# Performance work log

Measured on AMD Instinct MI355X. Metric: run time of the kernel, lower is better.

## Reference

```python
import jax, jax.numpy as jnp
import numpy as np

B, T, K, H = 8192, 96, 32, 768  # batch, max_len, output_dim (tags), bert hidden


def setup_inputs() -> dict:
    key = jax.random.key(0)
    k1, k2, k3, k4 = jax.random.split(key, 4)
    hidden = jax.random.normal(k1, (B, H), dtype=jnp.float32)
    target = jax.random.randint(k2, (B, T), 0, K, dtype=jnp.int32)
    # Dense(output_dim * max_len) params
    W = jax.random.normal(k3, (H, T * K), dtype=jnp.float32) * 0.02
    b = jnp.zeros((T * K,), dtype=jnp.float32)
    # tf.random.uniform transition matrix
    transitions = jax.random.uniform(k4, (K, K), dtype=jnp.float32)
    return {"hidden": hidden, "target": target, "W": W, "b": b, "transitions": transitions}


def _crf_log_norm(em_tm, transitions):
    # em_tm: [T, B, K] time-major emissions. Forward algorithm (logsumexp recurrence).
    def step(alpha, em_t):
        # alpha: [B, K]; broadcast over next-tag axis
        new = jax.nn.logsumexp(alpha[:, :, None] + transitions[None, :, :], axis=1) + em_t
        return new, None
    alpha, _ = jax.lax.scan(step, em_tm[0], em_tm[1:])
    return jax.nn.logsumexp(alpha, axis=-1)  # [B]


def _crf_sequence_score(em_btk, target, transitions):
    # unary: emission score at gold tags; binary: transition scores along gold path
    unary = jnp.take_along_axis(em_btk, target[..., None], axis=-1)[..., 0].sum(-1)
    binary = transitions[target[:, :-1], target[:, 1:]].sum(-1)
    return unary + binary  # [B]


def _viterbi_decode(em_tm, transitions):
    # em_tm: [T, B, K]. Max-product forward pass collecting backpointers.
    def fwd(v, em_t):
        scores = v[:, :, None] + transitions[None, :, :]  # [B, K_prev, K_next]
        bp = jnp.argmax(scores, axis=1).astype(jnp.int32)  # [B, K]
        return jnp.max(scores, axis=1) + em_t, bp
    v, bps = jax.lax.scan(fwd, em_tm[0], em_tm[1:])  # bps: [T-1, B, K]
    last_tag = jnp.argmax(v, axis=-1).astype(jnp.int32)  # [B]
    # backtrace (reverse scan); output index i is the tag at time i
    def back(tag, bp_t):
        prev = jnp.take_along_axis(bp_t, tag[:, None], axis=1)[:, 0]
        return prev, prev
    _, prevs = jax.lax.scan(back, last_tag, bps, reverse=True)  # [T-1, B]
    tags = jnp.concatenate([prevs, last_tag[None, :]], axis=0)  # [T, B]
    return jnp.transpose(tags), jnp.max(v, axis=-1)


def reference(hidden, target, W, b, transitions):
    # Dense with sigmoid, then reshape to (B, max_len, output_dim)
    em = jax.nn.sigmoid(hidden @ W + b).reshape(hidden.shape[0], T, K)
    em_tm = jnp.transpose(em, (1, 0, 2))  # time-major for scan
    log_likelihood = _crf_sequence_score(em, target, transitions) - _crf_log_norm(em_tm, transitions)
    decode_predict, _ = _viterbi_decode(em_tm, transitions)
    return decode_predict, log_likelihood
```

## Files before the change

### kernel.cpp

```cpp
#include <hip/hip_runtime.h>
#include <cstdint>
#include <cstddef>

#define B_  8192
#define T_  96
#define K_  32
#define H_  768
#define NK_ (T_ * K_)

typedef __attribute__((ext_vector_type(8))) _Float16 f16x8;
typedef __attribute__((ext_vector_type(4))) float    f32x4;

#define SCALE_UP   4096.0f
#define SCALE_DOWN (1.0f / 16777216.0f)

__device__ __forceinline__ void load_lds16(const void* g, void* l) {
    __builtin_amdgcn_global_load_lds(
        (const __attribute__((address_space(1))) unsigned int*)g,
        (__attribute__((address_space(3))) unsigned int*)l,
        16, 0, 0);
}

__global__ __launch_bounds__(256) void splitA_kernel(
    const float* __restrict__ A, _Float16* __restrict__ Ath, _Float16* __restrict__ Atl)
{
    const int g   = blockIdx.x * 256 + threadIdx.x;
    const int row = g / 96;
    const int o   = g - row * 96;
    const int ks  = o >> 2, qq = o & 3;
    const int r   = row & 127, rb = row >> 7;
    const size_t dst = (size_t)(rb * 24 + ks) * 4096 + r * 32 + ((qq ^ ((r >> 1) & 3)) << 3);

    f32x4 v0 = *(const f32x4*)(A + (size_t)row * H_ + o * 8);
    f32x4 v1 = *(const f32x4*)(A + (size_t)row * H_ + o * 8 + 4);
    f16x8 hi, lo;
#pragma unroll
    for (int e = 0; e < 8; e++) {
        float x = ((e < 4) ? v0[e] : v1[e - 4]) * SCALE_UP;
        _Float16 h = (_Float16)x;
        hi[e] = h;
        lo[e] = (_Float16)(x - (float)h);
    }
    *(f16x8*)&Ath[dst] = hi;
    *(f16x8*)&Atl[dst] = lo;
}

__global__ __launch_bounds__(256) void splitW_kernel(
    const float* __restrict__ W, _Float16* __restrict__ Wth, _Float16* __restrict__ Wtl)
{
    const int g   = blockIdx.x * 256 + threadIdx.x;
    const int ko  = g / NK_;
    const int col = g - ko * NK_;
    const int k0  = ko * 8;
    const int cb  = col >> 7, n = col & 127;
    const int ks  = k0 >> 5, qq = (k0 & 31) >> 3;
    const size_t dst = (size_t)(cb * 24 + ks) * 4096 + n * 32 + ((qq ^ ((n >> 1) & 3)) << 3);

    f16x8 hi, lo;
#pragma unroll
    for (int j = 0; j < 8; j++) {
        float x = W[(size_t)(k0 + j) * NK_ + col] * SCALE_UP;
        _Float16 h = (_Float16)x;
        hi[j] = h;
        lo[j] = (_Float16)(x - (float)h);
    }
    *(f16x8*)&Wth[dst] = hi;
    *(f16x8*)&Wtl[dst] = lo;
}

__global__ __launch_bounds__(256, 2) void gemm_mfma_sigmoid_kernel(
    const _Float16* __restrict__ Ath, const _Float16* __restrict__ Atl,
    const _Float16* __restrict__ Wth, const _Float16* __restrict__ Wtl,
    const float* __restrict__ bias, float* __restrict__ em)
{
    __shared__ _Float16 lds[2][4][4096];

    const int tid  = threadIdx.x;
    const int cb   = blockIdx.x;
    const int rb   = blockIdx.y;
    const int lane = tid & 63;
    const int w    = tid >> 6;
    const int wr   = w >> 1, wc = w & 1;
    const int fr   = lane & 15;
    const int kg   = lane >> 4;

    const _Float16* srcs[4] = {
        Ath + (size_t)(rb * 24) * 4096, Atl + (size_t)(rb * 24) * 4096,
        Wth + (size_t)(cb * 24) * 4096, Wtl + (size_t)(cb * 24) * 4096 };

    auto stage = [&](int ks, int bb) {
#pragma unroll
        for (int m = 0; m < 4; m++) {
            const _Float16* s = srcs[m] + (size_t)ks * 4096 + w * 1024 + lane * 8;
            _Float16* d = &lds[bb][m][w * 1024];
            load_lds16(s, d);
            load_lds16(s + 512, d + 512);
        }
    };

    f32x4 acc[4][4];
#pragma unroll
    for (int i = 0; i < 4; i++)
#pragma unroll
        for (int j = 0; j < 4; j++) acc[i][j] = (f32x4)0.0f;

    int cur = 0;
    stage(0, 0);

    for (int ks = 0; ks < 24; ks++) {
        __syncthreads();
        if (ks + 1 < 24) stage(ks + 1, cur ^ 1);

        f16x8 fah[4], fal[4], fbh[4], fbl[4];
#pragma unroll
        for (int mi = 0; mi < 4; mi++) {
            const int r   = wr * 64 + mi * 16 + fr;
            const int idx = r * 32 + ((kg ^ ((r >> 1) & 3)) << 3);
            fah[mi] = *(const f16x8*)&lds[cur][0][idx];
            fal[mi] = *(const f16x8*)&lds[cur][1][idx];
        }
#pragma unroll
        for (int ni = 0; ni < 4; ni++) {
            const int r   = wc * 64 + ni * 16 + fr;
            const int idx = r * 32 + ((kg ^ ((r >> 1) & 3)) << 3);
            fbh[ni] = *(const f16x8*)&lds[cur][2][idx];
            fbl[ni] = *(const f16x8*)&lds[cur][3][idx];
        }
#pragma unroll
        for (int mi = 0; mi < 4; mi++)
#pragma unroll
            for (int ni = 0; ni < 4; ni++) {
                acc[mi][ni] = __builtin_amdgcn_mfma_f32_16x16x32_f16(fah[mi], fbh[ni], acc[mi][ni], 0, 0, 0);
                acc[mi][ni] = __builtin_amdgcn_mfma_f32_16x16x32_f16(fah[mi], fbl[ni], acc[mi][ni], 0, 0, 0);
                acc[mi][ni] = __builtin_amdgcn_mfma_f32_16x16x32_f16(fal[mi], fbh[ni], acc[mi][ni], 0, 0, 0);
            }
        cur ^= 1;
    }

    const int er = rb * 128 + wr * 64 + (lane >> 4) * 4;
    const int ec = cb * 128 + wc * 64 + fr;
#pragma unroll
    for (int ni = 0; ni < 4; ni++) {
        const int   gc = ec + ni * 16;
        const float bv = bias[gc];
#pragma unroll
        for (int mi = 0; mi < 4; mi++)
#pragma unroll
            for (int r = 0; r < 4; r++) {
                const int gr = er + mi * 16 + r;
                float x = acc[mi][ni][r] * SCALE_DOWN + bv;
                em[(size_t)gr * NK_ + gc] = 1.0f / (1.0f + __expf(-x));
            }
    }
}

__global__ __launch_bounds__(256) void crf_scan_kernel(
    const float* __restrict__ em,
    const int* __restrict__ target,
    const float* __restrict__ trans,
    float* __restrict__ out_tags,
    float* __restrict__ ll)
{
    __shared__ float  trans_s[K_ * K_];
    __shared__ float4 ev4[8][16];
    __shared__ unsigned int bp_s[8][24][K_];

    const int tid = threadIdx.x;
    const int g   = tid >> 5;
    const int k   = tid & 31;
    const int b   = blockIdx.x * 8 + g;

    for (int i = tid; i < K_ * K_; i += 256) trans_s[i] = trans[i];
    __syncthreads();

    float tcol[K_], Ecol[K_];
#pragma unroll
    for (int p = 0; p < K_; p++) {
        tcol[p] = trans_s[p * K_ + k];
        Ecol[p] = __expf(tcol[p]);
    }

    const float* emb = em + (size_t)b * NK_;

    const float em0 = emb[k];
    float alpha = em0;
    float v     = em0;
    int   tgt_prev = target[b * T_];
    float unary  = (k == tgt_prev) ? em0 : 0.0f;
    float binary = 0.0f;
    unsigned int bpw = 0;

    float2* evp = (float2*)&ev4[g][0];

    for (int t = 1; t < T_; t++) {
        const float em_t = emb[t * K_ + k];

        float mh = alpha;
#pragma unroll
        for (int d = 16; d >= 1; d >>= 1) mh = fmaxf(mh, __shfl_xor(mh, d));
        const float e = __expf(alpha - mh);

        evp[k] = make_float2(e, v);
        __builtin_amdgcn_wave_barrier();

        float sum = 0.0f;
        float bv  = -1e30f;
        int   bi  = 0;
#pragma unroll
        for (int c = 0; c < 16; c++) {
            f32x4 q = *(const f32x4*)&ev4[g][c];
            const int p0 = 2 * c, p1 = 2 * c + 1;
            sum = fmaf(q[0], Ecol[p0], sum);
            float sv0 = q[1] + tcol[p0];
            if (sv0 > bv) { bv = sv0; bi = p0; }
            sum = fmaf(q[2], Ecol[p1], sum);
            float sv1 = q[3] + tcol[p1];
            if (sv1 > bv) { bv = sv1; bi = p1; }
        }

        alpha = mh + __logf(sum) + em_t;
        v     = bv + em_t;

        bpw |= (unsigned int)bi << (8 * ((t - 1) & 3));
        if (((t - 1) & 3) == 3) { bp_s[g][(t - 1) >> 2][k] = bpw; bpw = 0; }

        const int tgt = target[b * T_ + t];
        unary  += (k == tgt) ? em_t : 0.0f;
        binary += trans_s[tgt_prev * K_ + tgt];
        tgt_prev = tgt;
    }
    bp_s[g][23][k] = bpw;
    __builtin_amdgcn_wave_barrier();

    float m2 = alpha;
#pragma unroll
    for (int d = 16; d >= 1; d >>= 1) m2 = fmaxf(m2, __shfl_xor(m2, d));
    float s2 = __expf(alpha - m2);
#pragma unroll
    for (int d = 16; d >= 1; d >>= 1) s2 += __shfl_xor(s2, d);
    const float logZ = m2 + __logf(s2);

    float un = unary;
#pragma unroll
    for (int d = 16; d >= 1; d >>= 1) un += __shfl_xor(un, d);

    float bvv = v;
    int   bii = k;
#pragma unroll
    for (int d = 16; d >= 1; d >>= 1) {
        float ov = __shfl_xor(bvv, d);
        int   oi = __shfl_xor(bii, d);
        if (ov > bvv || (ov == bvv && oi < bii)) { bvv = ov; bii = oi; }
    }

    if (k == 0) {
        ll[b] = un + binary - logZ;
        float* ot = out_tags + (size_t)b * T_;
        int tag = bii;
        ot[T_ - 1] = (float)tag;
        for (int t = T_ - 2; t >= 0; t--) {
            unsigned int wd = bp_s[g][t >> 2][tag];
            tag = (wd >> (8 * (t & 3))) & 0xFF;
            ot[t] = (float)tag;
        }
    }
}

extern "C" void kernel_launch(void* const* d_in, const int* in_sizes, int n_in,
                              void* d_out, int out_size, void* d_ws, size_t ws_size,
                              hipStream_t stream)
{
    const float* hidden = (const float*)d_in[0];
    const int*   target = (const int*)d_in[1];
    const float* W      = (const float*)d_in[2];
    const float* bias   = (const float*)d_in[3];
    const float* trans  = (const float*)d_in[4];

    float* out      = (float*)d_out;
    float* out_tags = out;
    float* out_ll   = out + (size_t)B_ * T_;

    char* ws = (char*)d_ws;
    const size_t emB = (size_t)B_ * NK_ * 4;
    const size_t ahB = (size_t)B_ * H_ * 2;
    const size_t whB = (size_t)H_ * NK_ * 2;
    float*    em  = (float*)ws;
    _Float16* Ath = (_Float16*)(ws + emB);
    _Float16* Atl = (_Float16*)(ws + emB + ahB);
    _Float16* Wth = (_Float16*)(ws + emB + 2 * ahB);
    _Float16* Wtl = (_Float16*)(ws + emB + 2 * ahB + whB);

    splitA_kernel<<<(B_ * 96) / 256, 256, 0, stream>>>(hidden, Ath, Atl);
    splitW_kernel<<<(NK_ * 96) / 256, 256, 0, stream>>>(W, Wth, Wtl);

    dim3 gemm_grid(NK_ / 128, B_ / 128);
    gemm_mfma_sigmoid_kernel<<<gemm_grid, 256, 0, stream>>>(Ath, Atl, Wth, Wtl, bias, em);

    crf_scan_kernel<<<B_ / 8, 256, 0, stream>>>(em, target, trans, out_tags, out_ll);
}
```

Baseline: 300.8 us.

## Drop per-step max reduction in CRF forward via fixed offset renormalization

Removes the per-timestep wavefront max shuffle reduction from the logsumexp forward recurrence. Each step subtracts a constant 4 and the running value is rebased to lane 0 every 16 steps, with the accumulated offset added back at the end. It also computes the gold-path score in parallel across lanes before the scan, prefetches the next emission, and uses packed f32 FMA/add for the inner loops. This shortens the serial dependency chain per step, but overflow or underflow protection now depends on the sigmoid-bounded emissions and the transition range.

New measurement: 271.9 us. 1.11x faster.

```diff
diff --git a/kernel.cpp b/kernel.cpp
--- a/kernel.cpp
+++ b/kernel.cpp
@@ -10,6 +10,7 @@
 
 typedef __attribute__((ext_vector_type(8))) _Float16 f16x8;
 typedef __attribute__((ext_vector_type(4))) float    f32x4;
+typedef __attribute__((ext_vector_type(2))) float    f32x2;
 
 #define SCALE_UP   4096.0f
 #define SCALE_DOWN (1.0f / 16777216.0f)
@@ -19,6 +20,17 @@
         (const __attribute__((address_space(1))) unsigned int*)g,
         (__attribute__((address_space(3))) unsigned int*)l,
         16, 0, 0);
+}
+
+__device__ __forceinline__ f32x2 pk_add(f32x2 a, f32x2 b) {
+    f32x2 d;
+    asm("v_pk_add_f32 %0, %1, %2" : "=v"(d) : "v"(a), "v"(b));
+    return d;
+}
+__device__ __forceinline__ f32x2 pk_fma(f32x2 a, f32x2 b, f32x2 c) {
+    f32x2 d;
+    asm("v_pk_fma_f32 %0, %1, %2, %3" : "=v"(d) : "v"(a), "v"(b), "v"(c));
+    return d;
 }
 
 __global__ __launch_bounds__(256) void splitA_kernel(
@@ -162,8 +174,10 @@
     float* __restrict__ ll)
 {
     __shared__ float  trans_s[K_ * K_];
-    __shared__ float4 ev4[8][16];
+    __shared__ float  e_s[8][K_];
+    __shared__ float  v_s[8][K_];
     __shared__ unsigned int bp_s[8][24][K_];
+    __shared__ unsigned char tgt_s[8][T_];
 
     const int tid = threadIdx.x;
     const int g   = tid >> 5;
@@ -173,76 +187,99 @@
     for (int i = tid; i < K_ * K_; i += 256) trans_s[i] = trans[i];
     __syncthreads();
 
-    float tcol[K_], Ecol[K_];
-#pragma unroll
-    for (int p = 0; p < K_; p++) {
-        tcol[p] = trans_s[p * K_ + k];
-        Ecol[p] = __expf(tcol[p]);
-    }
-
-    const float* emb = em + (size_t)b * NK_;
-
-    const float em0 = emb[k];
-    float alpha = em0;
-    float v     = em0;
-    int   tgt_prev = target[b * T_];
-    float unary  = (k == tgt_prev) ? em0 : 0.0f;
-    float binary = 0.0f;
+    f32x2 t2[16], E2[16];
+#pragma unroll
+    for (int c = 0; c < 16; c++) {
+        float a0 = trans_s[(2 * c) * K_ + k];
+        float a1 = trans_s[(2 * c + 1) * K_ + k];
+        t2[c] = (f32x2){a0, a1};
+        E2[c] = (f32x2){__expf(a0), __expf(a1)};
+    }
+
+    const float* emb = em + (size_t)b * NK_ + k;
+
+    const int tg0 = target[b * T_ + k];
+    const int tg1 = target[b * T_ + 32 + k];
+    const int tg2 = target[b * T_ + 64 + k];
+    tgt_s[g][k] = (unsigned char)tg0;
+    tgt_s[g][k + 32] = (unsigned char)tg1;
+    tgt_s[g][k + 64] = (unsigned char)tg2;
+    __builtin_amdgcn_wave_barrier();
+
+    const float* emrow = em + (size_t)b * NK_;
+    float sc = emrow[k * K_ + tg0] + emrow[(k + 32) * K_ + tg1] + emrow[(k + 64) * K_ + tg2];
+    if (k > 0) sc += trans_s[(int)tgt_s[g][k - 1] * K_ + tg0];
+    sc += trans_s[(int)tgt_s[g][k + 31] * K_ + tg1];
+    sc += trans_s[(int)tgt_s[g][k + 63] * K_ + tg2];
+
+    const float em0 = emb[0];
+    float beta = em0;
+    float v    = em0;
+    float Cr   = 0.0f;
     unsigned int bpw = 0;
 
-    float2* evp = (float2*)&ev4[g][0];
-
-    for (int t = 1; t < T_; t++) {
-        const float em_t = emb[t * K_ + k];
-
-        float mh = alpha;
-#pragma unroll
-        for (int d = 16; d >= 1; d >>= 1) mh = fmaxf(mh, __shfl_xor(mh, d));
-        const float e = __expf(alpha - mh);
-
-        evp[k] = make_float2(e, v);
+    float em_t = emb[1 * K_];
+
+    auto STEP = [&](int t, int sh) {
+        float em_n = emb[(t + 1) * K_];
+        float e = __expf(beta);
+        e_s[g][k] = e;
+        v_s[g][k] = v;
         __builtin_amdgcn_wave_barrier();
 
-        float sum = 0.0f;
-        float bv  = -1e30f;
-        int   bi  = 0;
-#pragma unroll
-        for (int c = 0; c < 16; c++) {
-            f32x4 q = *(const f32x4*)&ev4[g][c];
-            const int p0 = 2 * c, p1 = 2 * c + 1;
-            sum = fmaf(q[0], Ecol[p0], sum);
-            float sv0 = q[1] + tcol[p0];
-            if (sv0 > bv) { bv = sv0; bi = p0; }
-            sum = fmaf(q[2], Ecol[p1], sum);
-            float sv1 = q[3] + tcol[p1];
-            if (sv1 > bv) { bv = sv1; bi = p1; }
-        }
-
-        alpha = mh + __logf(sum) + em_t;
-        v     = bv + em_t;
-
-        bpw |= (unsigned int)bi << (8 * ((t - 1) & 3));
-        if (((t - 1) & 3) == 3) { bp_s[g][(t - 1) >> 2][k] = bpw; bpw = 0; }
-
-        const int tgt = target[b * T_ + t];
-        unary  += (k == tgt) ? em_t : 0.0f;
-        binary += trans_s[tgt_prev * K_ + tgt];
-        tgt_prev = tgt;
-    }
+        f32x2 acc = (f32x2){0.0f, 0.0f};
+        float bv = -1e30f;
+        int   bi = 0;
+#pragma unroll
+        for (int q = 0; q < 8; q++) {
+            f32x4 eq = *(const f32x4*)&e_s[g][q * 4];
+            f32x4 vq = *(const f32x4*)&v_s[g][q * 4];
+            acc = pk_fma((f32x2){eq.x, eq.y}, E2[2 * q], acc);
+            acc = pk_fma((f32x2){eq.z, eq.w}, E2[2 * q + 1], acc);
+            f32x2 svA = pk_add((f32x2){vq.x, vq.y}, t2[2 * q]);
+            f32x2 svB = pk_add((f32x2){vq.z, vq.w}, t2[2 * q + 1]);
+            {
+                float wv = (svA.y > svA.x) ? svA.y : svA.x;
+                int   wi = (svA.y > svA.x) ? (4 * q + 1) : (4 * q);
+                if (wv > bv) { bv = wv; bi = wi; }
+            }
+            {
+                float wv = (svB.y > svB.x) ? svB.y : svB.x;
+                int   wi = (svB.y > svB.x) ? (4 * q + 3) : (4 * q + 2);
+                if (wv > bv) { bv = wv; bi = wi; }
+            }
+        }
+        float sum = acc.x + acc.y;
+        beta = __logf(sum) + (em_t - 4.0f);
+        v    = bv + em_t;
+        bpw |= (unsigned int)bi << (8 * sh);
+        if (sh == 3) { bp_s[g][(t - 1) >> 2][k] = bpw; bpw = 0; }
+        em_t = em_n;
+    };
+
+    for (int tb = 1; tb <= 89; tb += 4) {
+        STEP(tb, 0); STEP(tb + 1, 1); STEP(tb + 2, 2); STEP(tb + 3, 3);
+        if ((tb & 15) == 13) {
+            float d = __shfl(beta, 0, 32);
+            beta -= d;
+            Cr += d;
+        }
+    }
+    STEP(93, 0); STEP(94, 1); STEP(95, 2);
     bp_s[g][23][k] = bpw;
     __builtin_amdgcn_wave_barrier();
 
-    float m2 = alpha;
+    float m2 = beta;
 #pragma unroll
     for (int d = 16; d >= 1; d >>= 1) m2 = fmaxf(m2, __shfl_xor(m2, d));
-    float s2 = __expf(alpha - m2);
+    float s2 = __expf(beta - m2);
 #pragma unroll
     for (int d = 16; d >= 1; d >>= 1) s2 += __shfl_xor(s2, d);
-    const float logZ = m2 + __logf(s2);
-
-    float un = unary;
-#pragma unroll
-    for (int d = 16; d >= 1; d >>= 1) un += __shfl_xor(un, d);
+    const float logZ = 380.0f + Cr + m2 + __logf(s2);
+
+    float scr = sc;
+#pragma unroll
+    for (int d = 16; d >= 1; d >>= 1) scr += __shfl_xor(scr, d);
 
     float bvv = v;
     int   bii = k;
@@ -254,7 +291,7 @@
     }
 
     if (k == 0) {
-        ll[b] = un + binary - logZ;
+        ll[b] = scr - logZ;
         float* ot = out_tags + (size_t)b * T_;
         int tag = bii;
         ot[T_ - 1] = (float)tag;
```

## Rewrite CRF scan in exp-domain with 16 lanes per sequence and prefetching

Applied to the files above, without the earlier changes.

The CRF forward/Viterbi kernel now gives each sequence 16 lanes that each own two tags, so a block covers 16 sequences. The forward recurrence runs in the exponential domain with periodic power-of-two renormalization, which removes the per-step max reduction and log. Emissions are prefetched three steps ahead in registers. Backpointers are packed six per word at 5 bits each, and the gold-path score is computed in parallel up front. This halves the lane count and cuts transcendental and shuffle work per step, at the cost of more registers and some numerical risk from the fixed offset and renormalization.

Result: slower. 315.5 us (+4.9%).

```diff
diff --git a/kernel.cpp b/kernel.cpp
--- a/kernel.cpp
+++ b/kernel.cpp
@@ -154,7 +154,54 @@
     }
 }
 
-__global__ __launch_bounds__(256) void crf_scan_kernel(
+
+#define CRF_STEP(SH, R, WI)                                                  \
+  {                                                                          \
+    const float cem_a = pna[R], cem_b = pnb[R];                              \
+    pna[R] = *pfA; pnb[R] = *pfB; pfA += K_; pfB += K_;                      \
+    evg[l]      = make_float2(Ea, va);                                       \
+    evg[l + 16] = make_float2(Eb, vb);                                       \
+    __builtin_amdgcn_wave_barrier();                                         \
+    float fa = 0.0f, fb = 0.0f;                                              \
+    float bva = -1e30f, bvb = -1e30f;                                        \
+    int   bia = 0, bib = 0;                                                  \
+    _Pragma("unroll")                                                        \
+    for (int q = 0; q < 16; q++) {                                           \
+      f32x4 u = *(const f32x4*)&evg[2 * q];               \
+      const int p0 = 2 * q, p1 = 2 * q + 1;                                  \
+      float s;                                                               \
+      fa = fmaf(u[0], Ea2[p0], fa);  fb = fmaf(u[0], Eb2[p0], fb);           \
+      s = u[1] + tca[p0]; if (s > bva) { bva = s; bia = p0; }                \
+      s = u[1] + tcb[p0]; if (s > bvb) { bvb = s; bib = p0; }                \
+      fa = fmaf(u[2], Ea2[p1], fa);  fb = fmaf(u[2], Eb2[p1], fb);           \
+      s = u[3] + tca[p1]; if (s > bva) { bva = s; bia = p1; }                \
+      s = u[3] + tcb[p1]; if (s > bvb) { bvb = s; bib = p1; }                \
+    }                                                                        \
+    Ea = fa * __expf(cem_a - 4.0f);                                          \
+    Eb = fb * __expf(cem_b - 4.0f);                                          \
+    va = bva + cem_a;  vb = bvb + cem_b;                                     \
+    bpwa |= (unsigned int)bia << (5 * (SH));                                 \
+    bpwb |= (unsigned int)bib << (5 * (SH));                                 \
+    if ((SH) == 5) {                                                         \
+      bp5g[l * 17 + (WI)]        = bpwa;                                     \
+      bp5g[(l + 16) * 17 + (WI)] = bpwb;                                     \
+      bpwa = 0; bpwb = 0;                                                    \
+    }                                                                        \
+    __builtin_amdgcn_wave_barrier();                                         \
+  }
+
+#define CRF_RENORM()                                                         \
+  {                                                                          \
+    float m_ = fmaxf(Ea, Eb);                                                \
+    _Pragma("unroll")                                                        \
+    for (int d_ = 8; d_ >= 1; d_ >>= 1) m_ = fmaxf(m_, __shfl_xor(m_, d_));  \
+    const unsigned int eb_ = (__float_as_uint(m_) >> 23) & 255u;             \
+    const float s_ = __uint_as_float((254u - eb_) << 23);                    \
+    Ea *= s_; Eb *= s_;                                                      \
+    expo_sum += (int)eb_ - 127;                                              \
+  }
+
+__global__ __launch_bounds__(256, 2) void crf_scan_v5_kernel(
     const float* __restrict__ em,
     const int* __restrict__ target,
     const float* __restrict__ trans,
@@ -162,105 +209,106 @@
     float* __restrict__ ll)
 {
     __shared__ float  trans_s[K_ * K_];
-    __shared__ float4 ev4[8][16];
-    __shared__ unsigned int bp_s[8][24][K_];
+    __shared__ __align__(16) float2 ev[16][50];
+    __shared__ unsigned int bp5[16 * 545];
+    __shared__ unsigned char tgt_s[16][T_];
 
     const int tid = threadIdx.x;
-    const int g   = tid >> 5;
-    const int k   = tid & 31;
-    const int b   = blockIdx.x * 8 + g;
+    const int g   = tid >> 4;
+    const int l   = tid & 15;
+    const int b   = blockIdx.x * 16 + g;
 
     for (int i = tid; i < K_ * K_; i += 256) trans_s[i] = trans[i];
     __syncthreads();
 
-    float tcol[K_], Ecol[K_];
+    float tca[K_], tcb[K_], Ea2[K_], Eb2[K_];
 #pragma unroll
     for (int p = 0; p < K_; p++) {
-        tcol[p] = trans_s[p * K_ + k];
-        Ecol[p] = __expf(tcol[p]);
+        tca[p] = trans_s[p * K_ + l];
+        tcb[p] = trans_s[p * K_ + l + 16];
+        Ea2[p] = __expf(tca[p]);
+        Eb2[p] = __expf(tcb[p]);
     }
 
     const float* emb = em + (size_t)b * NK_;
-
-    const float em0 = emb[k];
-    float alpha = em0;
-    float v     = em0;
-    int   tgt_prev = target[b * T_];
-    float unary  = (k == tgt_prev) ? em0 : 0.0f;
-    float binary = 0.0f;
-    unsigned int bpw = 0;
-
-    float2* evp = (float2*)&ev4[g][0];
-
-    for (int t = 1; t < T_; t++) {
-        const float em_t = emb[t * K_ + k];
-
-        float mh = alpha;
-#pragma unroll
-        for (int d = 16; d >= 1; d >>= 1) mh = fmaxf(mh, __shfl_xor(mh, d));
-        const float e = __expf(alpha - mh);
-
-        evp[k] = make_float2(e, v);
-        __builtin_amdgcn_wave_barrier();
-
-        float sum = 0.0f;
-        float bv  = -1e30f;
-        int   bi  = 0;
-#pragma unroll
-        for (int c = 0; c < 16; c++) {
-            f32x4 q = *(const f32x4*)&ev4[g][c];
-            const int p0 = 2 * c, p1 = 2 * c + 1;
-            sum = fmaf(q[0], Ecol[p0], sum);
-            float sv0 = q[1] + tcol[p0];
-            if (sv0 > bv) { bv = sv0; bi = p0; }
-            sum = fmaf(q[2], Ecol[p1], sum);
-            float sv1 = q[3] + tcol[p1];
-            if (sv1 > bv) { bv = sv1; bi = p1; }
-        }
-
-        alpha = mh + __logf(sum) + em_t;
-        v     = bv + em_t;
-
-        bpw |= (unsigned int)bi << (8 * ((t - 1) & 3));
-        if (((t - 1) & 3) == 3) { bp_s[g][(t - 1) >> 2][k] = bpw; bpw = 0; }
-
-        const int tgt = target[b * T_ + t];
-        unary  += (k == tgt) ? em_t : 0.0f;
-        binary += trans_s[tgt_prev * K_ + tgt];
-        tgt_prev = tgt;
-    }
-    bp_s[g][23][k] = bpw;
+    float2*       evg  = &ev[g][0];
+    unsigned int* bp5g = &bp5[g * 545];
+
+    int tg[6];
+#pragma unroll
+    for (int j = 0; j < 6; j++) {
+        tg[j] = target[b * T_ + l + 16 * j];
+        tgt_s[g][l + 16 * j] = (unsigned char)tg[j];
+    }
     __builtin_amdgcn_wave_barrier();
-
-    float m2 = alpha;
-#pragma unroll
-    for (int d = 16; d >= 1; d >>= 1) m2 = fmaxf(m2, __shfl_xor(m2, d));
-    float s2 = __expf(alpha - m2);
-#pragma unroll
-    for (int d = 16; d >= 1; d >>= 1) s2 += __shfl_xor(s2, d);
-    const float logZ = m2 + __logf(s2);
-
-    float un = unary;
-#pragma unroll
-    for (int d = 16; d >= 1; d >>= 1) un += __shfl_xor(un, d);
-
-    float bvv = v;
-    int   bii = k;
-#pragma unroll
-    for (int d = 16; d >= 1; d >>= 1) {
-        float ov = __shfl_xor(bvv, d);
-        int   oi = __shfl_xor(bii, d);
-        if (ov > bvv || (ov == bvv && oi < bii)) { bvv = ov; bii = oi; }
-    }
-
-    if (k == 0) {
-        ll[b] = un + binary - logZ;
+    float gold = 0.0f;
+#pragma unroll
+    for (int j = 0; j < 6; j++) {
+        const int t = l + 16 * j;
+        gold += emb[t * K_ + tg[j]];
+        if (t > 0) gold += trans_s[(int)tgt_s[g][t - 1] * K_ + tg[j]];
+    }
+
+    const float em_a0 = emb[l];
+    const float em_b0 = emb[l + 16];
+    float Ea = __expf(em_a0), Eb = __expf(em_b0);
+    float va = em_a0,         vb = em_b0;
+    int   expo_sum = 0;
+    unsigned int bpwa = 0, bpwb = 0;
+
+    float pna[3], pnb[3];
+#pragma unroll
+    for (int j = 0; j < 3; j++) {
+        pna[j] = emb[(1 + j) * K_ + l];
+        pnb[j] = emb[(1 + j) * K_ + l + 16];
+    }
+    const float* pfA = emb + 4 * K_ + l;
+    const float* pfB = pfA + 16;
+
+    for (int it = 0; it < 15; ++it) {
+        CRF_STEP(0, 0, it)
+        CRF_STEP(1, 1, it)
+        CRF_STEP(2, 2, it)
+        CRF_STEP(3, 0, it)
+        CRF_STEP(4, 1, it)
+        CRF_STEP(5, 2, it)
+        if (it & 1) CRF_RENORM();
+    }
+    CRF_STEP(0, 0, 15)
+    CRF_STEP(1, 1, 15)
+    CRF_STEP(2, 2, 15)
+    CRF_STEP(3, 0, 15)
+    CRF_STEP(4, 1, 15)
+    bp5g[l * 17 + 15]        = bpwa;
+    bp5g[(l + 16) * 17 + 15] = bpwb;
+    __builtin_amdgcn_wave_barrier();
+
+    float S = Ea + Eb;
+#pragma unroll
+    for (int d = 8; d >= 1; d >>= 1) S += __shfl_xor(S, d);
+    const float logZ = __logf(S) + 380.0f + (float)expo_sum * 0.69314718055994531f;
+
+    float gsum = gold;
+#pragma unroll
+    for (int d = 8; d >= 1; d >>= 1) gsum += __shfl_xor(gsum, d);
+
+    float bv = va; int bi = l;
+    if (vb > bv) { bv = vb; bi = l + 16; }
+#pragma unroll
+    for (int d = 8; d >= 1; d >>= 1) {
+        float ov = __shfl_xor(bv, d);
+        int   oi = __shfl_xor(bi, d);
+        if (ov > bv || (ov == bv && oi < bi)) { bv = ov; bi = oi; }
+    }
+
+    if (l == 0) {
+        ll[b] = gsum - logZ;
         float* ot = out_tags + (size_t)b * T_;
-        int tag = bii;
+        int tag = bi;
         ot[T_ - 1] = (float)tag;
         for (int t = T_ - 2; t >= 0; t--) {
-            unsigned int wd = bp_s[g][t >> 2][tag];
-            tag = (wd >> (8 * (t & 3))) & 0xFF;
+            unsigned int wd = bp5g[tag * 17 + t / 6];
+            tag = (int)((wd >> (5 * (t % 6))) & 31u);
             ot[t] = (float)tag;
         }
     }
@@ -284,6 +332,7 @@
     const size_t emB = (size_t)B_ * NK_ * 4;
     const size_t ahB = (size_t)B_ * H_ * 2;
     const size_t whB = (size_t)H_ * NK_ * 2;
+
     float*    em  = (float*)ws;
     _Float16* Ath = (_Float16*)(ws + emB);
     _Float16* Atl = (_Float16*)(ws + emB + ahB);
@@ -296,5 +345,5 @@
     dim3 gemm_grid(NK_ / 128, B_ / 128);
     gemm_mfma_sigmoid_kernel<<<gemm_grid, 256, 0, stream>>>(Ath, Atl, Wth, Wtl, bias, em);
 
-    crf_scan_kernel<<<B_ / 8, 256, 0, stream>>>(em, target, trans, out_tags, out_ll);
-}
+    crf_scan_v5_kernel<<<B_ / 16, 256, 0, stream>>>(em, target, trans, out_tags, out_ll);
+}
```
